# Performance work log

Hardware: AMD Instinct MI355X
Metric: run time of the kernel (lower is better)

Reference implementation:

```python
import jax, jax.numpy as jnp
import numpy as np

# SequentialEdge (torchdrug): for each offset i in [-D, D], connect every atom of
# residue r to every atom of residue r+i within the same graph, keep only pairs on
# the same chain, relation id = i + D. We use a regular batch (B graphs, R residues
# per graph, A atoms per residue) so all shapes are static; edges filtered out by
# the same-chain test are padded with -1 rows (the torch original compacts them,
# which is a data-dependent shape and not jit-expressible).

B, R, A, D = 256, 256, 8, 2  # graphs, residues/graph, atoms/residue, max_distance
N = B * R * A
RTOT = B * R


def setup_inputs() -> dict:
    key = jax.random.key(0)
    atom2residue = jnp.arange(N, dtype=jnp.int32) // A        # [N]
    residue2graph = jnp.arange(RTOT, dtype=jnp.int32) // R    # [RTOT]
    chain_id = jax.random.randint(key, (RTOT,), 0, 4, dtype=jnp.int32)  # 4 chains/graph
    return {
        "chain_id": chain_id,
        "atom2residue": atom2residue,
        "residue2graph": residue2graph,
        "num_graph": B,
        "residues_per_graph": R,
        "atoms_per_residue": A,
        "max_distance": D,
    }


def reference(chain_id, atom2residue, residue2graph, num_graph, residues_per_graph,
              atoms_per_residue, max_distance):
    Bg, Rr, Aa, Dd = num_graph, residues_per_graph, atoms_per_residue, max_distance
    a = jnp.arange(Aa, dtype=jnp.int32)
    g = jnp.arange(Bg, dtype=jnp.int32)
    chunks = []
    for i in range(-Dd, Dd + 1):  # small fixed loop over 2*D+1 relation offsets
        Rv = Rr - abs(i)
        lo = max(0, -i)  # first valid local residue index for node_in
        local_in = jnp.arange(lo, lo + Rv, dtype=jnp.int32)           # [Rv]
        res_in = g[:, None] * Rr + local_in[None, :]                   # [B, Rv] global residue ids
        res_out = res_in + i                                           # partner residue, same graph
        node_in = res_in[..., None] * Aa + a                           # [B, Rv, A]
        node_out = res_out[..., None] * Aa + a                         # [B, Rv, A]
        # variadic_meshgrid order: in-atom varies slowly, out-atom fast, per residue segment
        ni = jnp.broadcast_to(node_in[..., :, None], (Bg, Rv, Aa, Aa)).reshape(-1)
        no = jnp.broadcast_to(node_out[..., None, :], (Bg, Rv, Aa, Aa)).reshape(-1)
        same_chain = chain_id[atom2residue[ni]] == chain_id[atom2residue[no]]
        rel = jnp.full(ni.shape, i + Dd, dtype=jnp.int32)
        edges = jnp.stack([ni, no, rel], axis=-1)                      # [E_i, 3]
        chunks.append(jnp.where(same_chain[:, None], edges, jnp.int32(-1)))
    edge_list = jnp.concatenate(chunks, axis=0)                        # [E_total, 3]
    return edge_list, jnp.int32(2 * Dd + 1)
```

## Files before the change

### kernel.cpp

```cpp
#include <hip/hip_runtime.h>
#include <hip/hip_bf16.h>


#define E_TOTAL   20873216u
#define INT_TOTAL 62619648u

typedef int v4i __attribute__((ext_vector_type(4)));

__global__ __launch_bounds__(256)
void seqedge_kernel(const int* __restrict__ chain, int* __restrict__ out) {
    __shared__ int lds[3200];
    const unsigned tid = threadIdx.x;
    const unsigned gid = blockIdx.x * 256u + tid;
    const unsigned e0  = gid * 4u;

    unsigned g, rem; int i, lo, rel;
    if (e0 < 4161536u)       { g = e0 / 16256u;                    rem = e0 - g * 16256u; i = -2; lo = 2; rel = 0; }
    else if (e0 < 8339456u)  { unsigned eo = e0 - 4161536u;  g = eo / 16320u; rem = eo - g * 16320u; i = -1; lo = 1; rel = 1; }
    else if (e0 < 12533760u) { unsigned eo = e0 - 8339456u;  g = eo >> 14;    rem = eo & 16383u;     i = 0;  lo = 0; rel = 2; }
    else if (e0 < 16711680u) { unsigned eo = e0 - 12533760u; g = eo / 16320u; rem = eo - g * 16320u; i = 1;  lo = 0; rel = 3; }
    else                     { unsigned eo = e0 - 16711680u; g = eo / 16256u; rem = eo - g * 16256u; i = 2;  lo = 0; rel = 4; }

    const unsigned rl  = (rem >> 6) + (unsigned)lo;
    const unsigned ai  = (rem >> 3) & 7u;
    const unsigned ao0 = rem & 7u;
    const int res_in  = (int)(g * 256u + rl);
    const int res_out = res_in + i;
    const bool same = chain[res_in] == chain[res_out];

    const int x  = same ? res_in * 8 + (int)ai : -1;
    const int r  = same ? rel : -1;
    const int yb = res_out * 8 + (int)ao0;
    const int y0 = same ? yb     : -1;
    const int y1 = same ? yb + 1 : -1;
    const int y2 = same ? yb + 2 : -1;
    const int y3 = same ? yb + 3 : -1;

    const unsigned wbase = 12u * tid + 16u * (tid >> 5) + 4u * ((tid >> 3) & 3u);
    v4i* ldsv = reinterpret_cast<v4i*>(&lds[wbase]);
    ldsv[0] = (v4i){x,  y0, r,  x};
    ldsv[1] = (v4i){y1, r,  x,  y2};
    ldsv[2] = (v4i){r,  x,  y3, r};

    __syncthreads();

    const unsigned out_base = blockIdx.x * 768u;
    v4i* outv = reinterpret_cast<v4i*>(out);
    #pragma unroll
    for (unsigned s = 0; s < 3; ++s) {
        const unsigned m    = s * 256u + tid;
        const unsigned c    = m / 3u;
        const unsigned rsub = m - c * 3u;
        const unsigned pb   = 12u * c + 16u * (c >> 5) + 4u * ((c >> 3) & 3u) + 4u * rsub;
        __builtin_nontemporal_store(*reinterpret_cast<const v4i*>(&lds[pb]),
                                    &outv[out_base + m]);
    }

    if (gid == 0u) out[INT_TOTAL] = 5;
}

extern "C" void kernel_launch(void* const* d_in, const int* in_sizes, int n_in,
                              void* d_out, int out_size, void* d_ws, size_t ws_size,
                              hipStream_t stream) {
    const int* chain_id = (const int*)d_in[0];
    int* out = (int*)d_out;
    seqedge_kernel<<<20384, 256, 0, stream>>>(chain_id, out);
}
```

Measured before the change: 259.8 us.

## Use persistent blocks looping over tiles with double-buffered LDS staging

Launches a fixed grid of blocks, each iterating over several output tiles, instead of one block per tile. LDS is double-buffered so one barrier per iteration is enough, and the per-thread gather offsets are computed once up front. Stores switch from nontemporal to ordinary stores. This trims block launch overhead and repeated index math, at the cost of less parallelism in flight per tile and possibly more cache pollution from the regular stores.

```diff
diff --git a/kernel.cpp b/kernel.cpp
--- a/kernel.cpp
+++ b/kernel.cpp
@@ -4,59 +4,70 @@
 
 #define E_TOTAL   20873216u
 #define INT_TOTAL 62619648u
+#define NBLOCKS   2548u
+#define NITER     8u
 
 typedef int v4i __attribute__((ext_vector_type(4)));
 
 __global__ __launch_bounds__(256)
 void seqedge_kernel(const int* __restrict__ chain, int* __restrict__ out) {
-    __shared__ int lds[3200];
+    __shared__ int lds[2][3200];
     const unsigned tid = threadIdx.x;
-    const unsigned gid = blockIdx.x * 256u + tid;
-    const unsigned e0  = gid * 4u;
-
-    unsigned g, rem; int i, lo, rel;
-    if (e0 < 4161536u)       { g = e0 / 16256u;                    rem = e0 - g * 16256u; i = -2; lo = 2; rel = 0; }
-    else if (e0 < 8339456u)  { unsigned eo = e0 - 4161536u;  g = eo / 16320u; rem = eo - g * 16320u; i = -1; lo = 1; rel = 1; }
-    else if (e0 < 12533760u) { unsigned eo = e0 - 8339456u;  g = eo >> 14;    rem = eo & 16383u;     i = 0;  lo = 0; rel = 2; }
-    else if (e0 < 16711680u) { unsigned eo = e0 - 12533760u; g = eo / 16320u; rem = eo - g * 16320u; i = 1;  lo = 0; rel = 3; }
-    else                     { unsigned eo = e0 - 16711680u; g = eo / 16256u; rem = eo - g * 16256u; i = 2;  lo = 0; rel = 4; }
-
-    const unsigned rl  = (rem >> 6) + (unsigned)lo;
-    const unsigned ai  = (rem >> 3) & 7u;
-    const unsigned ao0 = rem & 7u;
-    const int res_in  = (int)(g * 256u + rl);
-    const int res_out = res_in + i;
-    const bool same = chain[res_in] == chain[res_out];
-
-    const int x  = same ? res_in * 8 + (int)ai : -1;
-    const int r  = same ? rel : -1;
-    const int yb = res_out * 8 + (int)ao0;
-    const int y0 = same ? yb     : -1;
-    const int y1 = same ? yb + 1 : -1;
-    const int y2 = same ? yb + 2 : -1;
-    const int y3 = same ? yb + 3 : -1;
+    v4i* outv = reinterpret_cast<v4i*>(out);
 
     const unsigned wbase = 12u * tid + 16u * (tid >> 5) + 4u * ((tid >> 3) & 3u);
-    v4i* ldsv = reinterpret_cast<v4i*>(&lds[wbase]);
-    ldsv[0] = (v4i){x,  y0, r,  x};
-    ldsv[1] = (v4i){y1, r,  x,  y2};
-    ldsv[2] = (v4i){r,  x,  y3, r};
 
-    __syncthreads();
-
-    const unsigned out_base = blockIdx.x * 768u;
-    v4i* outv = reinterpret_cast<v4i*>(out);
+    unsigned pb[3], mm[3];
     #pragma unroll
     for (unsigned s = 0; s < 3; ++s) {
-        const unsigned m    = s * 256u + tid;
-        const unsigned c    = m / 3u;
-        const unsigned rsub = m - c * 3u;
-        const unsigned pb   = 12u * c + 16u * (c >> 5) + 4u * ((c >> 3) & 3u) + 4u * rsub;
-        __builtin_nontemporal_store(*reinterpret_cast<const v4i*>(&lds[pb]),
-                                    &outv[out_base + m]);
+        const unsigned m = s * 256u + tid;
+        const unsigned c = m / 3u;
+        const unsigned r = m - c * 3u;
+        pb[s] = 12u * c + 16u * (c >> 5) + 4u * ((c >> 3) & 3u) + 4u * r;
+        mm[s] = m;
     }
 
-    if (gid == 0u) out[INT_TOTAL] = 5;
+    for (unsigned it = 0; it < NITER; ++it) {
+        const unsigned tile = blockIdx.x + NBLOCKS * it;
+        const unsigned e0   = (tile * 256u + tid) * 4u;
+
+        unsigned g, rem; int i, lo, rel;
+        if (e0 < 4161536u)       { g = e0 / 16256u;                    rem = e0 - g * 16256u; i = -2; lo = 2; rel = 0; }
+        else if (e0 < 8339456u)  { unsigned eo = e0 - 4161536u;  g = eo / 16320u; rem = eo - g * 16320u; i = -1; lo = 1; rel = 1; }
+        else if (e0 < 12533760u) { unsigned eo = e0 - 8339456u;  g = eo >> 14;    rem = eo & 16383u;     i = 0;  lo = 0; rel = 2; }
+        else if (e0 < 16711680u) { unsigned eo = e0 - 12533760u; g = eo / 16320u; rem = eo - g * 16320u; i = 1;  lo = 0; rel = 3; }
+        else                     { unsigned eo = e0 - 16711680u; g = eo / 16256u; rem = eo - g * 16256u; i = 2;  lo = 0; rel = 4; }
+
+        const unsigned rl  = (rem >> 6) + (unsigned)lo;
+        const unsigned ai  = (rem >> 3) & 7u;
+        const unsigned ao0 = rem & 7u;
+        const int res_in  = (int)(g * 256u + rl);
+        const int res_out = res_in + i;
+        const bool same = chain[res_in] == chain[res_out];
+
+        const int x  = same ? res_in * 8 + (int)ai : -1;
+        const int r  = same ? rel : -1;
+        const int yb = res_out * 8 + (int)ao0;
+        const int y0 = same ? yb     : -1;
+        const int y1 = same ? yb + 1 : -1;
+        const int y2 = same ? yb + 2 : -1;
+        const int y3 = same ? yb + 3 : -1;
+
+        int* buf = lds[it & 1u];
+        v4i* ldsv = reinterpret_cast<v4i*>(&buf[wbase]);
+        ldsv[0] = (v4i){x,  y0, r,  x};
+        ldsv[1] = (v4i){y1, r,  x,  y2};
+        ldsv[2] = (v4i){r,  x,  y3, r};
+
+        __syncthreads();
+
+        const unsigned out_base = tile * 768u;
+        #pragma unroll
+        for (unsigned s = 0; s < 3; ++s)
+            outv[out_base + mm[s]] = *reinterpret_cast<const v4i*>(&buf[pb[s]]);
+    }
+
+    if (blockIdx.x == 0u && tid == 0u) out[INT_TOTAL] = 5;
 }
 
 extern "C" void kernel_launch(void* const* d_in, const int* in_sizes, int n_in,
@@ -64,5 +75,5 @@
                               hipStream_t stream) {
     const int* chain_id = (const int*)d_in[0];
     int* out = (int*)d_out;
-    seqedge_kernel<<<20384, 256, 0, stream>>>(chain_id, out);
+    seqedge_kernel<<<NBLOCKS, 256, 0, stream>>>(chain_id, out);
 }
```

New measurement: 252.0 us. 3.0% less time.
